# Kernel tuning notes

Hardware: AMD Instinct MI355X
Metric: run time of the kernel (lower is better)

The kernel has to match this reference:

```python
import jax, jax.numpy as jnp
import numpy as np

DT_ALPHA = 3.0
TW_ALPHA = 2.0
MAX_ITER = 5000
STOP_THR = 0.005
SINK_EPS = 1e-16
RECON_EPS = 1e-12


def pairwise_euclidean_distance(x, y):
    return jnp.sum(x * x, axis=1, keepdims=True) + jnp.sum(y * y, axis=1) - 2.0 * (x @ y.T)


def sinkhorn(M, a, b, alpha):
    # Faithful port of ETP.forward: K = exp(-alpha*M), alternating u/v scaling,
    # error checked every 50 iterations (at cpt % 50 == 1).
    K = jnp.exp(-M * alpha)
    n = a.shape[0]
    u0 = jnp.ones_like(a) / n
    v0 = jnp.zeros_like(b)

    def cond(state):
        u, v, err, cpt = state
        return (err > STOP_THR) & (cpt < MAX_ITER)

    def body(state):
        u, v, err, cpt = state
        v = b / (K.T @ u + SINK_EPS)
        u = a / (K @ v + SINK_EPS)
        cpt = cpt + 1
        err = jax.lax.cond(
            cpt % 50 == 1,
            lambda: jnp.sum(jnp.abs(v * (K.T @ u) - b)),  # inf-norm of a [1]-vector
            lambda: err,
        )
        return (u, v, err, cpt)

    u, v, _, _ = jax.lax.while_loop(
        cond, body, (u0, v0, jnp.asarray(1.0, M.dtype), jnp.asarray(0, jnp.int32))
    )
    transp = u * (K * v.T)
    loss = jnp.sum(transp * M)
    return loss, transp


def setup_inputs() -> dict:
    key = jax.random.key(0)
    kd, kw, kt, kb = jax.random.split(key, 4)
    N, V, K, E = 4096, 10000, 100, 384

    def l2norm(x):
        return x / jnp.linalg.norm(x, axis=1, keepdims=True)

    doc_embeddings = l2norm(jax.random.normal(kd, (N, E), dtype=jnp.float32))
    word_embeddings = l2norm(jax.random.normal(kw, (V, E), dtype=jnp.float32))
    topic_embeddings = l2norm(jax.random.normal(kt, (K, E), dtype=jnp.float32) * 0.1)
    train_bow = jax.random.uniform(kb, (N, V), dtype=jnp.float32)
    word_weights = jnp.ones((V, 1), dtype=jnp.float32) / V
    topic_weights = jnp.ones((K, 1), dtype=jnp.float32) / K
    return {
        "train_bow": train_bow,
        "doc_embeddings": doc_embeddings,
        "word_embeddings": word_embeddings,
        "topic_embeddings": topic_embeddings,
        "word_weights": word_weights,
        "topic_weights": topic_weights,
    }


def reference(train_bow, doc_embeddings, word_embeddings, topic_embeddings,
              word_weights, topic_weights):
    N = doc_embeddings.shape[0]
    K = topic_embeddings.shape[0]

    # Doc-Topic transport: a uniform over docs, b = softmax(topic_weights)
    M_dt = pairwise_euclidean_distance(doc_embeddings, topic_embeddings)
    a_dt = jnp.ones((N, 1), dtype=M_dt.dtype) / N
    b_dt = jax.nn.softmax(topic_weights, axis=0)
    loss_DT, transp_DT = sinkhorn(M_dt, a_dt, b_dt, DT_ALPHA)

    # Topic-Word transport: a uniform over topics, b = softmax(word_weights)
    M_tw = pairwise_euclidean_distance(topic_embeddings, word_embeddings)
    a_tw = jnp.ones((K, 1), dtype=M_tw.dtype) / K
    b_tw = jax.nn.softmax(word_weights, axis=0)
    loss_TW, transp_TW = sinkhorn(M_tw, a_tw, b_tw, TW_ALPHA)

    theta = transp_DT * N        # [N, K]
    beta = transp_TW * K         # [K, V]
    recon = theta @ beta         # [N, V]
    loss_DSR = -jnp.mean(jnp.sum(train_bow * jnp.log(recon + RECON_EPS), axis=1))
    return loss_DSR + loss_DT + loss_TW
```

## Files before the change

### kernel.cpp

```cpp
#include <hip/hip_runtime.h>

#define N_DOCS   4096
#define N_WORDS  10000
#define N_TOPICS 100
#define EDIM     384
#define KPAD     128
#define BT_ROWS  10112
#define RECON_BLOCKS (79 * 32)
#define APPLY_BLOCKS 2088

#define OFF_KDT   16u
#define OFF_KDTT  (OFF_KDT  + 409600u)
#define OFF_KTW   (OFF_KDTT + 409600u)
#define OFF_BDT   (OFF_KTW  + 1000000u)
#define OFF_BTW   (OFF_BDT  + 128u)
#define OFF_ND    (OFF_BTW  + 10016u)
#define OFF_NW    (OFF_ND   + 4096u)
#define OFF_NT    (OFF_NW   + 10016u)
#define OFF_UDT   (OFF_NT   + 128u)
#define OFF_VDT   (OFF_UDT  + 4096u)
#define OFF_UTW   (OFF_VDT  + 128u)
#define OFF_VTW   (OFF_UTW  + 128u)
#define OFF_THB   (OFF_VTW  + 10016u)
#define OFF_BTT   (OFF_THB  + 262144u)
#define OFF_RPART (OFF_BTT  + 647168u)
#define OFF_APART (OFF_RPART + 5056u)

typedef __attribute__((ext_vector_type(8))) short bf16x8;
typedef __attribute__((ext_vector_type(4))) float f32x4;

__device__ __forceinline__ float block_reduce_sum_256(float v, volatile float* sh) {
#pragma unroll
  for (int off = 32; off > 0; off >>= 1) v += __shfl_down(v, off, 64);
  __syncthreads();
  if ((threadIdx.x & 63) == 0) sh[threadIdx.x >> 6] = v;
  __syncthreads();
  return sh[0] + sh[1] + sh[2] + sh[3];
}

__device__ __forceinline__ float block_reduce_sum_1024(float v, volatile float* sh) {
#pragma unroll
  for (int off = 32; off > 0; off >>= 1) v += __shfl_down(v, off, 64);
  if ((threadIdx.x & 63) == 0) sh[threadIdx.x >> 6] = v;
  __syncthreads();
  if (threadIdx.x == 0) {
    float s = 0.f;
    for (int i = 0; i < 16; ++i) s += sh[i];
    sh[16] = s;
  }
  __syncthreads();
  float r = sh[16];
  __syncthreads();
  return r;
}

__device__ __forceinline__ float block_reduce_max_1024(float v, volatile float* sh) {
#pragma unroll
  for (int off = 32; off > 0; off >>= 1) v = fmaxf(v, __shfl_down(v, off, 64));
  if ((threadIdx.x & 63) == 0) sh[threadIdx.x >> 6] = v;
  __syncthreads();
  if (threadIdx.x == 0) {
    float m = sh[0];
    for (int i = 1; i < 16; ++i) m = fmaxf(m, sh[i]);
    sh[16] = m;
  }
  __syncthreads();
  float r = sh[16];
  __syncthreads();
  return r;
}

__device__ __forceinline__ unsigned short f2bf(float x) {
  union { float f; unsigned int u; } c; c.f = x;
  unsigned int r = c.u + 0x7FFF + ((c.u >> 16) & 1);
  return (unsigned short)(r >> 16);
}

__global__ __launch_bounds__(1024)
void prep_norms_kernel(const float* __restrict__ docs, const float* __restrict__ words,
                       const float* __restrict__ topics,
                       const float* __restrict__ topic_w, const float* __restrict__ word_w,
                       float* __restrict__ nd, float* __restrict__ nw, float* __restrict__ nt,
                       float* __restrict__ b_dt, float* __restrict__ b_tw,
                       float* __restrict__ errs) {
  int tid = threadIdx.x, lane = tid & 63, wave = tid >> 6;
  if (blockIdx.x < 888) {
    int row = blockIdx.x * 16 + wave;
    if (row < N_DOCS + N_WORDS + N_TOPICS) {
      const float* src; float* dst; int r;
      if (row < N_DOCS)                { src = docs;   r = row;                    dst = nd; }
      else if (row < N_DOCS + N_WORDS) { src = words;  r = row - N_DOCS;           dst = nw; }
      else                             { src = topics; r = row - N_DOCS - N_WORDS; dst = nt; }
      float s = 0.f;
#pragma unroll
      for (int k = lane; k < EDIM; k += 64) { float x = src[r * EDIM + k]; s += x * x; }
#pragma unroll
      for (int off = 32; off > 0; off >>= 1) s += __shfl_down(s, off, 64);
      if (lane == 0) dst[r] = s;
    }
    return;
  }
  __shared__ float sh[20];
  float m = (tid < N_TOPICS) ? topic_w[tid] : -3.0e38f;
  m = block_reduce_max_1024(m, sh);
  float e = (tid < N_TOPICS) ? __expf(topic_w[tid] - m) : 0.f;
  float s = block_reduce_sum_1024(e, sh);
  if (tid < N_TOPICS) b_dt[tid] = e / s;
  float m2 = -3.0e38f;
  for (int i = tid * 4; i < N_WORDS; i += 4096) {
    float4 w = *reinterpret_cast<const float4*>(&word_w[i]);
    m2 = fmaxf(fmaxf(m2, fmaxf(w.x, w.y)), fmaxf(w.z, w.w));
  }
  m2 = block_reduce_max_1024(m2, sh);
  float s2 = 0.f;
  for (int i = tid * 4; i < N_WORDS; i += 4096) {
    float4 w = *reinterpret_cast<const float4*>(&word_w[i]);
    s2 += __expf(w.x - m2) + __expf(w.y - m2) + __expf(w.z - m2) + __expf(w.w - m2);
  }
  s2 = block_reduce_sum_1024(s2, sh);
  float inv2 = 1.0f / s2;
  for (int i = tid * 4; i < N_WORDS; i += 4096) {
    float4 w = *reinterpret_cast<const float4*>(&word_w[i]);
    float4 o = make_float4(__expf(w.x - m2) * inv2, __expf(w.y - m2) * inv2,
                           __expf(w.z - m2) * inv2, __expf(w.w - m2) * inv2);
    *reinterpret_cast<float4*>(&b_tw[i]) = o;
  }
  if (tid < 2) errs[tid] = 0.f;
}

__global__ __launch_bounds__(256)
void dist_kernel(const float* __restrict__ docs, const float* __restrict__ words,
                 const float* __restrict__ topics,
                 const float* __restrict__ nd, const float* __restrict__ nw,
                 const float* __restrict__ nt,
                 float* __restrict__ Kdt, float* __restrict__ KdtT,
                 float* __restrict__ Ktw) {
  __shared__ __align__(16) float As[16][64];
  __shared__ __align__(16) float Bs[16][64];
  const int bid = blockIdx.x;
  const float *A, *B, *nA, *nB; float *Kout, *KoutT; int nI, nJ, i0, j0; float alpha;
  if (bid < 128) {
    A = docs; B = topics; nA = nd; nB = nt; Kout = Kdt; KoutT = KdtT;
    nI = N_DOCS; nJ = N_TOPICS; alpha = 3.0f;
    j0 = (bid & 1) * 64; i0 = (bid >> 1) * 64;
  } else {
    int b2 = bid - 128;
    A = topics; B = words; nA = nt; nB = nw; Kout = Ktw; KoutT = nullptr;
    nI = N_TOPICS; nJ = N_WORDS; alpha = 2.0f;
    i0 = (b2 & 1) * 64; j0 = (b2 >> 1) * 64;
  }
  const int tid = threadIdx.x;
  const int r = tid & 63, kg = tid >> 6;
  const int tx = tid & 15, ty = tid >> 4;
  float acc[4][4] = {};
  for (int k0 = 0; k0 < EDIM; k0 += 16) {
    float4 av = make_float4(0.f, 0.f, 0.f, 0.f);
    float4 bv = make_float4(0.f, 0.f, 0.f, 0.f);
    int gi = i0 + r, gj = j0 + r;
    if (gi < nI) av = *reinterpret_cast<const float4*>(&A[gi * EDIM + k0 + kg * 4]);
    if (gj < nJ) bv = *reinterpret_cast<const float4*>(&B[gj * EDIM + k0 + kg * 4]);
    As[kg * 4 + 0][r] = av.x; As[kg * 4 + 1][r] = av.y;
    As[kg * 4 + 2][r] = av.z; As[kg * 4 + 3][r] = av.w;
    Bs[kg * 4 + 0][r] = bv.x; Bs[kg * 4 + 1][r] = bv.y;
    Bs[kg * 4 + 2][r] = bv.z; Bs[kg * 4 + 3][r] = bv.w;
    __syncthreads();
#pragma unroll
    for (int kk = 0; kk < 16; ++kk) {
      float4 a4 = *reinterpret_cast<const float4*>(&As[kk][ty * 4]);
      float4 b4 = *reinterpret_cast<const float4*>(&Bs[kk][tx * 4]);
      float aa[4] = {a4.x, a4.y, a4.z, a4.w};
      float bb[4] = {b4.x, b4.y, b4.z, b4.w};
#pragma unroll
      for (int di = 0; di < 4; ++di)
#pragma unroll
        for (int dj = 0; dj < 4; ++dj) acc[di][dj] += aa[di] * bb[dj];
    }
    __syncthreads();
  }
#pragma unroll
  for (int di = 0; di < 4; ++di) {
    int gi = i0 + ty * 4 + di;
    if (gi < nI) {
      float na = nA[gi];
#pragma unroll
      for (int dj = 0; dj < 4; ++dj) {
        int gj = j0 + tx * 4 + dj;
        if (gj < nJ) {
          float val = __expf(-alpha * (na + nB[gj] - 2.f * acc[di][dj]));
          Kout[(size_t)gi * nJ + gj] = val;
          if (KoutT) KoutT[(size_t)gj * nI + gi] = val;
        }
      }
    }
  }
}

__global__ __launch_bounds__(256)
void cs_kernel(const float* __restrict__ KdtT, const float* __restrict__ b_dt,
               float* __restrict__ v_dt,
               const float* __restrict__ Ktw, const float* __restrict__ b_tw,
               float* __restrict__ v_tw) {
  __shared__ float sh[4];
  const int tid = threadIdx.x;
  if (blockIdx.x < 100) {
    int j = blockIdx.x;
    float s = 0.f;
#pragma unroll 8
    for (int i = tid; i < N_DOCS; i += 256) s += KdtT[(size_t)j * N_DOCS + i];
    s = block_reduce_sum_256(s, sh);
    if (tid == 0) v_dt[j] = b_dt[j] / (s * (1.0f / N_DOCS) + 1e-16f);
  } else {
    int j = (blockIdx.x - 100) * 256 + tid;
    if (j < N_WORDS) {
      float s = 0.f;
#pragma unroll 10
      for (int i = 0; i < N_TOPICS; ++i) s += Ktw[(size_t)i * N_WORDS + j];
      v_tw[j] = b_tw[j] / (s * 0.01f + 1e-16f);
    }
  }
}

__global__ __launch_bounds__(256)
void u_kernel(const float* __restrict__ Kdt, const float* __restrict__ v_dt,
              float* __restrict__ u_dt,
              const float* __restrict__ Ktw, const float* __restrict__ v_tw,
              float* __restrict__ u_tw) {
  __shared__ float vl[N_TOPICS];
  __shared__ float sh[4];
  const int tid = threadIdx.x;
  if (blockIdx.x < 16) {
    if (tid < N_TOPICS) vl[tid] = v_dt[tid];
    __syncthreads();
    int i = blockIdx.x * 256 + tid;
    float d = 0.f;
    const float* row = &Kdt[(size_t)i * N_TOPICS];
#pragma unroll
    for (int j4 = 0; j4 < N_TOPICS; j4 += 4) {
      float4 kv = *reinterpret_cast<const float4*>(&row[j4]);
      d += kv.x * vl[j4] + kv.y * vl[j4 + 1] + kv.z * vl[j4 + 2] + kv.w * vl[j4 + 3];
    }
    u_dt[i] = (1.0f / N_DOCS) / (d + 1e-16f);
  } else {
    int i = blockIdx.x - 16;
    float d = 0.f;
    const float* row = &Ktw[(size_t)i * N_WORDS];
    for (int j = tid * 4; j < N_WORDS; j += 1024) {
      float4 kv = *reinterpret_cast<const float4*>(&row[j]);
      float4 vv = *reinterpret_cast<const float4*>(&v_tw[j]);
      d += kv.x * vv.x + kv.y * vv.y + kv.z * vv.z + kv.w * vv.w;
    }
    d = block_reduce_sum_256(d, sh);
    if (tid == 0) u_tw[i] = 0.01f / (d + 1e-16f);
  }
}

__global__ __launch_bounds__(256)
void err_kernel(const float* __restrict__ KdtT, const float* __restrict__ u_dt,
                const float* __restrict__ v_dt, const float* __restrict__ b_dt,
                const float* __restrict__ Ktw, const float* __restrict__ u_tw,
                const float* __restrict__ v_tw, const float* __restrict__ b_tw,
                float* __restrict__ errs) {
  __shared__ float sh[4];
  __shared__ float ul[N_TOPICS];
  const int tid = threadIdx.x;
  if (blockIdx.x < 100) {
    int j = blockIdx.x;
    float s = 0.f;
#pragma unroll 8
    for (int i = tid; i < N_DOCS; i += 256) s += KdtT[(size_t)j * N_DOCS + i] * u_dt[i];
    s = block_reduce_sum_256(s, sh);
    if (tid == 0) atomicAdd(&errs[0], fabsf(v_dt[j] * s - b_dt[j]));
  } else {
    if (tid < N_TOPICS) ul[tid] = u_tw[tid];
    __syncthreads();
    int j = (blockIdx.x - 100) * 256 + tid;
    float e = 0.f;
    if (j < N_WORDS) {
      float s = 0.f;
#pragma unroll 10
      for (int i = 0; i < N_TOPICS; ++i) s += Ktw[(size_t)i * N_WORDS + j] * ul[i];
      e = fabsf(v_tw[j] * s - b_tw[j]);
    }
    e = block_reduce_sum_256(e, sh);
    if (tid == 0) atomicAdd(&errs[1], e);
  }
}

__global__ __launch_bounds__(1024)
void rem_kernel(const float* __restrict__ Kdt, const float* __restrict__ KdtT,
                const float* __restrict__ b_dt, float* __restrict__ u_dt,
                float* __restrict__ v_dt,
                const float* __restrict__ Ktw, const float* __restrict__ b_tw,
                float* __restrict__ u_tw, float* __restrict__ v_tw,
                const float* __restrict__ errs) {
  __shared__ float rsm[20104];
  const int tid = threadIdx.x, wave = tid >> 6, lane = tid & 63;
  if (blockIdx.x == 0) {
    float err = errs[0];
    if (!(err > 0.005f)) return;
    float* u_l = rsm; float* v_l = rsm + 4096; float* bl = rsm + 4196; float* esh = rsm + 4296;
    for (int i = tid; i < N_DOCS; i += 1024) u_l[i] = u_dt[i];
    if (tid < N_TOPICS) { bl[tid] = b_dt[tid]; v_l[tid] = v_dt[tid]; }
    __syncthreads();
    int cpt = 1;
    while (err > 0.005f && cpt < 5000) {
      for (int j = wave; j < N_TOPICS; j += 16) {
        float s = 0.f;
        for (int i = lane; i < N_DOCS; i += 64) s += KdtT[(size_t)j * N_DOCS + i] * u_l[i];
#pragma unroll
        for (int off = 32; off > 0; off >>= 1) s += __shfl_down(s, off, 64);
        if (lane == 0) v_l[j] = bl[j] / (s + 1e-16f);
      }
      __syncthreads();
      for (int i = tid; i < N_DOCS; i += 1024) {
        float d = 0.f;
        for (int j = 0; j < N_TOPICS; ++j) d += Kdt[(size_t)i * N_TOPICS + j] * v_l[j];
        u_l[i] = (1.0f / N_DOCS) / (d + 1e-16f);
      }
      __syncthreads();
      ++cpt;
      if (cpt % 50 == 1) {
        if (tid == 0) *esh = 0.f;
        __syncthreads();
        for (int j = wave; j < N_TOPICS; j += 16) {
          float s = 0.f;
          for (int i = lane; i < N_DOCS; i += 64) s += KdtT[(size_t)j * N_DOCS + i] * u_l[i];
#pragma unroll
          for (int off = 32; off > 0; off >>= 1) s += __shfl_down(s, off, 64);
          if (lane == 0) atomicAdd(esh, fabsf(v_l[j] * s - bl[j]));
        }
        __syncthreads();
        err = *esh;
        __syncthreads();
      }
    }
    for (int i = tid; i < N_DOCS; i += 1024) u_dt[i] = u_l[i];
    if (tid < N_TOPICS) v_dt[tid] = v_l[tid];
  } else {
    float err = errs[1];
    if (!(err > 0.005f)) return;
    float* v_l = rsm; float* bl = rsm + 10000; float* u_l = rsm + 20000; float* esh = rsm + 20100;
    for (int j = tid; j < N_WORDS; j += 1024) { v_l[j] = v_tw[j]; bl[j] = b_tw[j]; }
    if (tid < N_TOPICS) u_l[tid] = u_tw[tid];
    __syncthreads();
    int cpt = 1;
    while (err > 0.005f && cpt < 5000) {
      for (int j = tid; j < N_WORDS; j += 1024) {
        float s = 0.f;
        for (int i = 0; i < N_TOPICS; ++i) s += Ktw[(size_t)i * N_WORDS + j] * u_l[i];
        v_l[j] = bl[j] / (s + 1e-16f);
      }
      __syncthreads();
      for (int i = wave; i < N_TOPICS; i += 16) {
        float s = 0.f;
        for (int j = lane; j < N_WORDS; j += 64) s += Ktw[(size_t)i * N_WORDS + j] * v_l[j];
#pragma unroll
        for (int off = 32; off > 0; off >>= 1) s += __shfl_down(s, off, 64);
        if (lane == 0) u_l[i] = 0.01f / (s + 1e-16f);
      }
      __syncthreads();
      ++cpt;
      if (cpt % 50 == 1) {
        if (tid == 0) *esh = 0.f;
        __syncthreads();
        float e = 0.f;
        for (int j = tid; j < N_WORDS; j += 1024) {
          float s = 0.f;
          for (int i = 0; i < N_TOPICS; ++i) s += Ktw[(size_t)i * N_WORDS + j] * u_l[i];
          e += fabsf(v_l[j] * s - bl[j]);
        }
        atomicAdd(esh, e);
        __syncthreads();
        err = *esh;
        __syncthreads();
      }
    }
    for (int j = tid; j < N_WORDS; j += 1024) v_tw[j] = v_l[j];
    if (tid < N_TOPICS) u_tw[tid] = u_l[tid];
  }
}

__global__ __launch_bounds__(256)
void apply_kernel(const float* __restrict__ Kdt, const float* __restrict__ u_dt,
                  const float* __restrict__ v_dt,
                  const float* __restrict__ Ktw, const float* __restrict__ u_tw,
                  const float* __restrict__ v_tw,
                  unsigned short* __restrict__ theta_b, unsigned short* __restrict__ beta_bT,
                  double* __restrict__ apart) {
  __shared__ float sh[4];
  __shared__ float ul[N_TOPICS];
  const int tid = threadIdx.x;
  float lp = 0.f;
  if (blockIdx.x < 2048) {
    int idx = blockIdx.x * 256 + tid;
    int i = idx >> 7, k = idx & 127;
    unsigned short o = 0;
    if (k < N_TOPICS) {
      float kv = Kdt[(size_t)i * N_TOPICS + k];
      float t = u_dt[i] * kv * v_dt[k];
      lp = t * (-__logf(kv) * (1.0f / 3.0f));
      o = f2bf(t * (float)N_DOCS);
    }
    theta_b[idx] = o;
  } else {
    if (tid < N_TOPICS) ul[tid] = u_tw[tid];
    __syncthreads();
    int n = (blockIdx.x - 2048) * 256 + tid;
    if (n < N_WORDS) {
      float vn = v_tw[n];
      unsigned short* dst = &beta_bT[(size_t)n * KPAD];
#pragma unroll 2
      for (int kc = 0; kc < KPAD; kc += 8) {
        unsigned short pk[8];
#pragma unroll
        for (int q = 0; q < 8; ++q) {
          int k = kc + q;
          unsigned short o = 0;
          if (k < N_TOPICS) {
            float kv = Ktw[(size_t)k * N_WORDS + n];
            float t = ul[k] * kv * vn;
            lp += t * (-__logf(kv) * 0.5f);
            o = f2bf(t * (float)N_TOPICS);
          }
          pk[q] = o;
        }
        *(uint4*)&dst[kc] = *(uint4*)pk;
      }
    } else if (n < BT_ROWS) {
      unsigned short* dst = &beta_bT[(size_t)n * KPAD];
      uint4 z = make_uint4(0, 0, 0, 0);
#pragma unroll
      for (int kc = 0; kc < KPAD; kc += 8) *(uint4*)&dst[kc] = z;
    }
  }
  lp = block_reduce_sum_256(lp, sh);
  if (tid == 0) apart[blockIdx.x] = (double)lp;
}

#define AS_LD 136
#define CLD   132
__global__ __launch_bounds__(256, 2)
void recon_kernel(const unsigned short* __restrict__ theta_b,
                  const unsigned short* __restrict__ beta_bT,
                  const float* __restrict__ bow, double* __restrict__ rpart) {
  __shared__ __align__(16) char smem[128 * AS_LD * 2 * 2];
  __shared__ float sh4[4];
  unsigned short* As = (unsigned short*)smem;
  unsigned short* Bs = As + 128 * AS_LD;
  float* C = (float*)smem;
  const int tid = threadIdx.x;
  const int c0 = blockIdx.x * 128, r0 = blockIdx.y * 128;

#pragma unroll
  for (int pass = 0; pass < 8; ++pass) {
    int idx = pass * 256 + tid;
    int r = idx >> 4, k16 = idx & 15;
    *(uint4*)&As[r * AS_LD + k16 * 8] = *(const uint4*)&theta_b[(size_t)(r0 + r) * KPAD + k16 * 8];
    *(uint4*)&Bs[r * AS_LD + k16 * 8] = *(const uint4*)&beta_bT[(size_t)(c0 + r) * KPAD + k16 * 8];
  }
  __syncthreads();

  const int wave = tid >> 6, lane = tid & 63;
  const int wr = (wave >> 1) * 64, wc = (wave & 1) * 64;
  const int lm = lane & 15, q = lane >> 4;
  f32x4 acc[4][4] = {};
#pragma unroll
  for (int kc = 0; kc < 4; ++kc) {
    int k = kc * 32 + q * 8;
    bf16x8 af[4], bfr[4];
#pragma unroll
    for (int t = 0; t < 4; ++t) {
      af[t]  = *(const bf16x8*)&As[(wr + t * 16 + lm) * AS_LD + k];
      bfr[t] = *(const bf16x8*)&Bs[(wc + t * 16 + lm) * AS_LD + k];
    }
#pragma unroll
    for (int mi = 0; mi < 4; ++mi)
#pragma unroll
      for (int ni = 0; ni < 4; ++ni)
        acc[mi][ni] = __builtin_amdgcn_mfma_f32_16x16x32_bf16(af[mi], bfr[ni],
                                                              acc[mi][ni], 0, 0, 0);
  }
  __syncthreads();

#pragma unroll
  for (int mi = 0; mi < 4; ++mi)
#pragma unroll
    for (int ni = 0; ni < 4; ++ni)
#pragma unroll
      for (int reg = 0; reg < 4; ++reg) {
        int row = wr + mi * 16 + q * 4 + reg;
        int col = wc + ni * 16 + lm;
        C[row * CLD + col] = acc[mi][ni][reg];
      }
  __syncthreads();

  float lp = 0.f;
  const int c4 = tid & 31;
  const int rb = tid >> 5;
  const int gj0 = c0 + c4 * 4;
  if (gj0 < N_WORDS) {
#pragma unroll
    for (int it = 0; it < 16; ++it) {
      int row = rb + it * 8;
      float4 bw = *reinterpret_cast<const float4*>(&bow[(size_t)(r0 + row) * N_WORDS + gj0]);
      float4 rc = *reinterpret_cast<const float4*>(&C[row * CLD + c4 * 4]);
      lp += bw.x * __logf(rc.x + 1e-12f) + bw.y * __logf(rc.y + 1e-12f)
          + bw.z * __logf(rc.z + 1e-12f) + bw.w * __logf(rc.w + 1e-12f);
    }
  }
  lp = block_reduce_sum_256(lp, sh4);
  if (tid == 0) rpart[blockIdx.y * 79 + blockIdx.x] = (double)lp;
}

__global__ __launch_bounds__(1024)
void finalize_kernel(const double* __restrict__ rpart, const double* __restrict__ apart,
                     float* __restrict__ out) {
  __shared__ double sh[17];
  const int tid = threadIdx.x, lane = tid & 63;
  double s2 = 0.0, s01 = 0.0;
  for (int i = tid; i < RECON_BLOCKS; i += 1024) s2 += rpart[i];
  for (int i = tid; i < APPLY_BLOCKS; i += 1024) s01 += apart[i];
  double t = s01 - s2 * (1.0 / N_DOCS);
#pragma unroll
  for (int off = 32; off > 0; off >>= 1) t += __shfl_down(t, off, 64);
  if (lane == 0) sh[tid >> 6] = t;
  __syncthreads();
  if (tid == 0) {
    double s = 0.0;
    for (int i = 0; i < 16; ++i) s += sh[i];
    out[0] = (float)s;
  }
}

extern "C" void kernel_launch(void* const* d_in, const int* in_sizes, int n_in,
                              void* d_out, int out_size, void* d_ws, size_t ws_size,
                              hipStream_t stream) {
  const float* bow     = (const float*)d_in[0];
  const float* docs    = (const float*)d_in[1];
  const float* words   = (const float*)d_in[2];
  const float* topics  = (const float*)d_in[3];
  const float* word_w  = (const float*)d_in[4];
  const float* topic_w = (const float*)d_in[5];
  float* out = (float*)d_out;

  float* fws  = (float*)d_ws;
  float* errs = fws + 8;
  float* Kdt  = fws + OFF_KDT;
  float* KdtT = fws + OFF_KDTT;
  float* Ktw  = fws + OFF_KTW;
  float* b_dt = fws + OFF_BDT;
  float* b_tw = fws + OFF_BTW;
  float* nd   = fws + OFF_ND;
  float* nw   = fws + OFF_NW;
  float* nt   = fws + OFF_NT;
  float* u_dt = fws + OFF_UDT;
  float* v_dt = fws + OFF_VDT;
  float* u_tw = fws + OFF_UTW;
  float* v_tw = fws + OFF_VTW;
  unsigned short* theta_b = (unsigned short*)(fws + OFF_THB);
  unsigned short* beta_bT = (unsigned short*)(fws + OFF_BTT);
  double* rpart = (double*)(fws + OFF_RPART);
  double* apart = (double*)(fws + OFF_APART);

  prep_norms_kernel<<<dim3(889), dim3(1024), 0, stream>>>(
      docs, words, topics, topic_w, word_w, nd, nw, nt, b_dt, b_tw, errs);
  dist_kernel<<<dim3(442), dim3(256), 0, stream>>>(
      docs, words, topics, nd, nw, nt, Kdt, KdtT, Ktw);
  cs_kernel<<<dim3(140), dim3(256), 0, stream>>>(KdtT, b_dt, v_dt, Ktw, b_tw, v_tw);
  u_kernel<<<dim3(116), dim3(256), 0, stream>>>(Kdt, v_dt, u_dt, Ktw, v_tw, u_tw);
  err_kernel<<<dim3(140), dim3(256), 0, stream>>>(
      KdtT, u_dt, v_dt, b_dt, Ktw, u_tw, v_tw, b_tw, errs);
  rem_kernel<<<dim3(2), dim3(1024), 0, stream>>>(
      Kdt, KdtT, b_dt, u_dt, v_dt, Ktw, b_tw, u_tw, v_tw, errs);
  apply_kernel<<<dim3(APPLY_BLOCKS), dim3(256), 0, stream>>>(
      Kdt, u_dt, v_dt, Ktw, u_tw, v_tw, theta_b, beta_bT, apart);
  recon_kernel<<<dim3(79, 32), dim3(256), 0, stream>>>(theta_b, beta_bT, bow, rpart);
  finalize_kernel<<<dim3(1), dim3(1024), 0, stream>>>(rpart, apart, out);

  (void)in_sizes; (void)n_in; (void)out_size; (void)ws_size;
}
```

Baseline: 368.4 us.

## Fuse Sinkhorn stages into a cooperative kernel and compute distances with bf16 MFMA

The separate norm and softmax prep kernel is removed. Row norms are now computed inside the distance kernel, and the softmax weights are computed inside the Sinkhorn kernel. The distance GEMM switches from fp32 FMA tiling to bf16 MFMA, and the four Sinkhorn launches (column sums, u update, error check, remaining iterations) become one cooperative kernel separated by grid.sync. This is meant to cut launch overhead and an extra pass over the embeddings. In exchange, the dot products are computed in bf16, which adds error before the exponential. The iterative remainder loop now runs with 256 instead of 1024 threads per block, which could slow it down if many iterations execute.

```diff
diff --git a/kernel.cpp b/kernel.cpp
--- a/kernel.cpp
+++ b/kernel.cpp
@@ -1,4 +1,7 @@
 #include <hip/hip_runtime.h>
+#include <hip/hip_cooperative_groups.h>
+
+namespace cg = cooperative_groups;
 
 #define N_DOCS   4096
 #define N_WORDS  10000
@@ -14,10 +17,7 @@
 #define OFF_KTW   (OFF_KDTT + 409600u)
 #define OFF_BDT   (OFF_KTW  + 1000000u)
 #define OFF_BTW   (OFF_BDT  + 128u)
-#define OFF_ND    (OFF_BTW  + 10016u)
-#define OFF_NW    (OFF_ND   + 4096u)
-#define OFF_NT    (OFF_NW   + 10016u)
-#define OFF_UDT   (OFF_NT   + 128u)
+#define OFF_UDT   (OFF_BTW  + 10016u)
 #define OFF_VDT   (OFF_UDT  + 4096u)
 #define OFF_UTW   (OFF_VDT  + 128u)
 #define OFF_VTW   (OFF_UTW  + 128u)
@@ -38,36 +38,13 @@
   return sh[0] + sh[1] + sh[2] + sh[3];
 }
 
-__device__ __forceinline__ float block_reduce_sum_1024(float v, volatile float* sh) {
-#pragma unroll
-  for (int off = 32; off > 0; off >>= 1) v += __shfl_down(v, off, 64);
+__device__ __forceinline__ float block_reduce_max_256(float v, volatile float* sh) {
+#pragma unroll
+  for (int off = 32; off > 0; off >>= 1) v = fmaxf(v, __shfl_down(v, off, 64));
+  __syncthreads();
   if ((threadIdx.x & 63) == 0) sh[threadIdx.x >> 6] = v;
   __syncthreads();
-  if (threadIdx.x == 0) {
-    float s = 0.f;
-    for (int i = 0; i < 16; ++i) s += sh[i];
-    sh[16] = s;
-  }
-  __syncthreads();
-  float r = sh[16];
-  __syncthreads();
-  return r;
-}
-
-__device__ __forceinline__ float block_reduce_max_1024(float v, volatile float* sh) {
-#pragma unroll
-  for (int off = 32; off > 0; off >>= 1) v = fmaxf(v, __shfl_down(v, off, 64));
-  if ((threadIdx.x & 63) == 0) sh[threadIdx.x >> 6] = v;
-  __syncthreads();
-  if (threadIdx.x == 0) {
-    float m = sh[0];
-    for (int i = 1; i < 16; ++i) m = fmaxf(m, sh[i]);
-    sh[16] = m;
-  }
-  __syncthreads();
-  float r = sh[16];
-  __syncthreads();
-  return r;
+  return fmaxf(fmaxf(sh[0], sh[1]), fmaxf(sh[2], sh[3]));
 }
 
 __device__ __forceinline__ unsigned short f2bf(float x) {
@@ -76,204 +53,181 @@
   return (unsigned short)(r >> 16);
 }
 
-__global__ __launch_bounds__(1024)
-void prep_norms_kernel(const float* __restrict__ docs, const float* __restrict__ words,
-                       const float* __restrict__ topics,
-                       const float* __restrict__ topic_w, const float* __restrict__ word_w,
-                       float* __restrict__ nd, float* __restrict__ nw, float* __restrict__ nt,
-                       float* __restrict__ b_dt, float* __restrict__ b_tw,
-                       float* __restrict__ errs) {
-  int tid = threadIdx.x, lane = tid & 63, wave = tid >> 6;
-  if (blockIdx.x < 888) {
-    int row = blockIdx.x * 16 + wave;
-    if (row < N_DOCS + N_WORDS + N_TOPICS) {
-      const float* src; float* dst; int r;
-      if (row < N_DOCS)                { src = docs;   r = row;                    dst = nd; }
-      else if (row < N_DOCS + N_WORDS) { src = words;  r = row - N_DOCS;           dst = nw; }
-      else                             { src = topics; r = row - N_DOCS - N_WORDS; dst = nt; }
-      float s = 0.f;
-#pragma unroll
-      for (int k = lane; k < EDIM; k += 64) { float x = src[r * EDIM + k]; s += x * x; }
-#pragma unroll
-      for (int off = 32; off > 0; off >>= 1) s += __shfl_down(s, off, 64);
-      if (lane == 0) dst[r] = s;
-    }
-    return;
-  }
-  __shared__ float sh[20];
-  float m = (tid < N_TOPICS) ? topic_w[tid] : -3.0e38f;
-  m = block_reduce_max_1024(m, sh);
-  float e = (tid < N_TOPICS) ? __expf(topic_w[tid] - m) : 0.f;
-  float s = block_reduce_sum_1024(e, sh);
-  if (tid < N_TOPICS) b_dt[tid] = e / s;
-  float m2 = -3.0e38f;
-  for (int i = tid * 4; i < N_WORDS; i += 4096) {
-    float4 w = *reinterpret_cast<const float4*>(&word_w[i]);
-    m2 = fmaxf(fmaxf(m2, fmaxf(w.x, w.y)), fmaxf(w.z, w.w));
-  }
-  m2 = block_reduce_max_1024(m2, sh);
-  float s2 = 0.f;
-  for (int i = tid * 4; i < N_WORDS; i += 4096) {
-    float4 w = *reinterpret_cast<const float4*>(&word_w[i]);
-    s2 += __expf(w.x - m2) + __expf(w.y - m2) + __expf(w.z - m2) + __expf(w.w - m2);
-  }
-  s2 = block_reduce_sum_1024(s2, sh);
-  float inv2 = 1.0f / s2;
-  for (int i = tid * 4; i < N_WORDS; i += 4096) {
-    float4 w = *reinterpret_cast<const float4*>(&word_w[i]);
-    float4 o = make_float4(__expf(w.x - m2) * inv2, __expf(w.y - m2) * inv2,
-                           __expf(w.z - m2) * inv2, __expf(w.w - m2) * inv2);
-    *reinterpret_cast<float4*>(&b_tw[i]) = o;
-  }
-  if (tid < 2) errs[tid] = 0.f;
-}
-
+#define DLD 40
 __global__ __launch_bounds__(256)
 void dist_kernel(const float* __restrict__ docs, const float* __restrict__ words,
                  const float* __restrict__ topics,
-                 const float* __restrict__ nd, const float* __restrict__ nw,
-                 const float* __restrict__ nt,
                  float* __restrict__ Kdt, float* __restrict__ KdtT,
                  float* __restrict__ Ktw) {
-  __shared__ __align__(16) float As[16][64];
-  __shared__ __align__(16) float Bs[16][64];
-  const int bid = blockIdx.x;
-  const float *A, *B, *nA, *nB; float *Kout, *KoutT; int nI, nJ, i0, j0; float alpha;
+  __shared__ __align__(16) unsigned short Abf[64 * DLD];
+  __shared__ __align__(16) unsigned short Bbf[64 * DLD];
+  __shared__ float na[64], nb[64];
+  const int bid = blockIdx.x, tid = threadIdx.x;
+  const float *A, *B; float *Kout, *KoutT; int nI, nJ, i0, j0; float alpha;
   if (bid < 128) {
-    A = docs; B = topics; nA = nd; nB = nt; Kout = Kdt; KoutT = KdtT;
+    A = docs; B = topics; Kout = Kdt; KoutT = KdtT;
     nI = N_DOCS; nJ = N_TOPICS; alpha = 3.0f;
     j0 = (bid & 1) * 64; i0 = (bid >> 1) * 64;
   } else {
     int b2 = bid - 128;
-    A = topics; B = words; nA = nt; nB = nw; Kout = Ktw; KoutT = nullptr;
+    A = topics; B = words; Kout = Ktw; KoutT = nullptr;
     nI = N_TOPICS; nJ = N_WORDS; alpha = 2.0f;
     i0 = (b2 & 1) * 64; j0 = (b2 >> 1) * 64;
   }
-  const int tid = threadIdx.x;
-  const int r = tid & 63, kg = tid >> 6;
-  const int tx = tid & 15, ty = tid >> 4;
-  float acc[4][4] = {};
-  for (int k0 = 0; k0 < EDIM; k0 += 16) {
-    float4 av = make_float4(0.f, 0.f, 0.f, 0.f);
-    float4 bv = make_float4(0.f, 0.f, 0.f, 0.f);
-    int gi = i0 + r, gj = j0 + r;
-    if (gi < nI) av = *reinterpret_cast<const float4*>(&A[gi * EDIM + k0 + kg * 4]);
-    if (gj < nJ) bv = *reinterpret_cast<const float4*>(&B[gj * EDIM + k0 + kg * 4]);
-    As[kg * 4 + 0][r] = av.x; As[kg * 4 + 1][r] = av.y;
-    As[kg * 4 + 2][r] = av.z; As[kg * 4 + 3][r] = av.w;
-    Bs[kg * 4 + 0][r] = bv.x; Bs[kg * 4 + 1][r] = bv.y;
-    Bs[kg * 4 + 2][r] = bv.z; Bs[kg * 4 + 3][r] = bv.w;
-    __syncthreads();
-#pragma unroll
-    for (int kk = 0; kk < 16; ++kk) {
-      float4 a4 = *reinterpret_cast<const float4*>(&As[kk][ty * 4]);
-      float4 b4 = *reinterpret_cast<const float4*>(&Bs[kk][tx * 4]);
-      float aa[4] = {a4.x, a4.y, a4.z, a4.w};
-      float bb[4] = {b4.x, b4.y, b4.z, b4.w};
-#pragma unroll
-      for (int di = 0; di < 4; ++di)
-#pragma unroll
-        for (int dj = 0; dj < 4; ++dj) acc[di][dj] += aa[di] * bb[dj];
-    }
-    __syncthreads();
-  }
-#pragma unroll
-  for (int di = 0; di < 4; ++di) {
-    int gi = i0 + ty * 4 + di;
-    if (gi < nI) {
-      float na = nA[gi];
-#pragma unroll
-      for (int dj = 0; dj < 4; ++dj) {
-        int gj = j0 + tx * 4 + dj;
-        if (gj < nJ) {
-          float val = __expf(-alpha * (na + nB[gj] - 2.f * acc[di][dj]));
-          Kout[(size_t)gi * nJ + gj] = val;
-          if (KoutT) KoutT[(size_t)gj * nI + gi] = val;
-        }
+  const int rs = tid >> 3, c4 = tid & 7;
+  const int giA0 = i0 + rs, giA1 = i0 + rs + 32;
+  const int gjB0 = j0 + rs, gjB1 = j0 + rs + 32;
+  const int wave = tid >> 6, lane = tid & 63, lm = lane & 15, q = lane >> 4;
+  const int wr = wave * 16;
+  float ssA0 = 0.f, ssA1 = 0.f, ssB0 = 0.f, ssB1 = 0.f;
+  f32x4 acc[4] = {};
+  for (int kc = 0; kc < 12; ++kc) {
+    const int kb = kc * 32 + c4 * 4;
+    float4 a0 = make_float4(0.f, 0.f, 0.f, 0.f), a1 = a0, b0 = a0, b1 = a0;
+    if (giA0 < nI) a0 = *(const float4*)&A[(size_t)giA0 * EDIM + kb];
+    if (giA1 < nI) a1 = *(const float4*)&A[(size_t)giA1 * EDIM + kb];
+    if (gjB0 < nJ) b0 = *(const float4*)&B[(size_t)gjB0 * EDIM + kb];
+    if (gjB1 < nJ) b1 = *(const float4*)&B[(size_t)gjB1 * EDIM + kb];
+    ssA0 += a0.x * a0.x + a0.y * a0.y + a0.z * a0.z + a0.w * a0.w;
+    ssA1 += a1.x * a1.x + a1.y * a1.y + a1.z * a1.z + a1.w * a1.w;
+    ssB0 += b0.x * b0.x + b0.y * b0.y + b0.z * b0.z + b0.w * b0.w;
+    ssB1 += b1.x * b1.x + b1.y * b1.y + b1.z * b1.z + b1.w * b1.w;
+    ushort4 pa0 = make_ushort4(f2bf(a0.x), f2bf(a0.y), f2bf(a0.z), f2bf(a0.w));
+    ushort4 pa1 = make_ushort4(f2bf(a1.x), f2bf(a1.y), f2bf(a1.z), f2bf(a1.w));
+    ushort4 pb0 = make_ushort4(f2bf(b0.x), f2bf(b0.y), f2bf(b0.z), f2bf(b0.w));
+    ushort4 pb1 = make_ushort4(f2bf(b1.x), f2bf(b1.y), f2bf(b1.z), f2bf(b1.w));
+    __syncthreads();
+    *(ushort4*)&Abf[rs * DLD + c4 * 4]        = pa0;
+    *(ushort4*)&Abf[(rs + 32) * DLD + c4 * 4] = pa1;
+    *(ushort4*)&Bbf[rs * DLD + c4 * 4]        = pb0;
+    *(ushort4*)&Bbf[(rs + 32) * DLD + c4 * 4] = pb1;
+    __syncthreads();
+    bf16x8 af = *(const bf16x8*)&Abf[(wr + lm) * DLD + q * 8];
+#pragma unroll
+    for (int ni = 0; ni < 4; ++ni) {
+      bf16x8 bf = *(const bf16x8*)&Bbf[(ni * 16 + lm) * DLD + q * 8];
+      acc[ni] = __builtin_amdgcn_mfma_f32_16x16x32_bf16(af, bf, acc[ni], 0, 0, 0);
+    }
+  }
+  ssA0 += __shfl_down(ssA0, 4); ssA0 += __shfl_down(ssA0, 2); ssA0 += __shfl_down(ssA0, 1);
+  ssA1 += __shfl_down(ssA1, 4); ssA1 += __shfl_down(ssA1, 2); ssA1 += __shfl_down(ssA1, 1);
+  ssB0 += __shfl_down(ssB0, 4); ssB0 += __shfl_down(ssB0, 2); ssB0 += __shfl_down(ssB0, 1);
+  ssB1 += __shfl_down(ssB1, 4); ssB1 += __shfl_down(ssB1, 2); ssB1 += __shfl_down(ssB1, 1);
+  __syncthreads();
+  if ((tid & 7) == 0) {
+    na[rs] = ssA0; na[rs + 32] = ssA1;
+    nb[rs] = ssB0; nb[rs + 32] = ssB1;
+  }
+  __syncthreads();
+#pragma unroll
+  for (int ni = 0; ni < 4; ++ni) {
+    int col = ni * 16 + lm, gj = j0 + col;
+#pragma unroll
+    for (int reg = 0; reg < 4; ++reg) {
+      int row = wr + q * 4 + reg, gi = i0 + row;
+      if (gi < nI && gj < nJ) {
+        float d = na[row] + nb[col] - 2.f * acc[ni][reg];
+        float val = __expf(-alpha * d);
+        Kout[(size_t)gi * nJ + gj] = val;
+        if (KoutT) KoutT[(size_t)gj * nI + gi] = val;
       }
     }
   }
 }
 
 __global__ __launch_bounds__(256)
-void cs_kernel(const float* __restrict__ KdtT, const float* __restrict__ b_dt,
-               float* __restrict__ v_dt,
-               const float* __restrict__ Ktw, const float* __restrict__ b_tw,
-               float* __restrict__ v_tw) {
-  __shared__ float sh[4];
-  const int tid = threadIdx.x;
-  if (blockIdx.x < 100) {
-    int j = blockIdx.x;
+void sinkhorn_kernel(const float* __restrict__ Kdt, const float* __restrict__ KdtT,
+                     const float* __restrict__ Ktw,
+                     const float* __restrict__ topic_w, const float* __restrict__ word_w,
+                     float* __restrict__ b_dt, float* __restrict__ b_tw,
+                     float* __restrict__ u_dt, float* __restrict__ v_dt,
+                     float* __restrict__ u_tw, float* __restrict__ v_tw,
+                     float* __restrict__ errs) {
+  cg::grid_group grid = cg::this_grid();
+  __shared__ float rsm[20104];
+  const int bid = blockIdx.x, tid = threadIdx.x;
+  const int wave = tid >> 6, lane = tid & 63;
+
+  if (bid < 100) {
+    int j = bid;
+    float m = (tid < N_TOPICS) ? topic_w[tid] : -3.0e38f;
+    m = block_reduce_max_256(m, rsm);
+    float e = (tid < N_TOPICS) ? __expf(topic_w[tid] - m) : 0.f;
+    float S = block_reduce_sum_256(e, rsm);
     float s = 0.f;
 #pragma unroll 8
     for (int i = tid; i < N_DOCS; i += 256) s += KdtT[(size_t)j * N_DOCS + i];
-    s = block_reduce_sum_256(s, sh);
-    if (tid == 0) v_dt[j] = b_dt[j] / (s * (1.0f / N_DOCS) + 1e-16f);
+    s = block_reduce_sum_256(s, rsm);
+    if (tid == 0) {
+      float bj = __expf(topic_w[j] - m) / S;
+      b_dt[j] = bj;
+      v_dt[j] = bj / (s * (1.0f / N_DOCS) + 1e-16f);
+      if (j == 0) { errs[0] = 0.f; errs[1] = 0.f; }
+    }
   } else {
-    int j = (blockIdx.x - 100) * 256 + tid;
+    float m2 = -3.0e38f;
+    for (int i = tid * 4; i < N_WORDS; i += 1024) {
+      float4 w = *(const float4*)&word_w[i];
+      m2 = fmaxf(fmaxf(m2, fmaxf(w.x, w.y)), fmaxf(w.z, w.w));
+    }
+    m2 = block_reduce_max_256(m2, rsm);
+    float s2 = 0.f;
+    for (int i = tid * 4; i < N_WORDS; i += 1024) {
+      float4 w = *(const float4*)&word_w[i];
+      s2 += __expf(w.x - m2) + __expf(w.y - m2) + __expf(w.z - m2) + __expf(w.w - m2);
+    }
+    s2 = block_reduce_sum_256(s2, rsm);
+    int j = (bid - 100) * 256 + tid;
     if (j < N_WORDS) {
       float s = 0.f;
 #pragma unroll 10
       for (int i = 0; i < N_TOPICS; ++i) s += Ktw[(size_t)i * N_WORDS + j];
-      v_tw[j] = b_tw[j] / (s * 0.01f + 1e-16f);
-    }
-  }
-}
-
-__global__ __launch_bounds__(256)
-void u_kernel(const float* __restrict__ Kdt, const float* __restrict__ v_dt,
-              float* __restrict__ u_dt,
-              const float* __restrict__ Ktw, const float* __restrict__ v_tw,
-              float* __restrict__ u_tw) {
-  __shared__ float vl[N_TOPICS];
-  __shared__ float sh[4];
-  const int tid = threadIdx.x;
-  if (blockIdx.x < 16) {
+      float bj = __expf(word_w[j] - m2) / s2;
+      b_tw[j] = bj;
+      v_tw[j] = bj / (s * 0.01f + 1e-16f);
+    }
+  }
+  grid.sync();
+
+  if (bid < 16) {
+    float* vl = rsm + 4;
     if (tid < N_TOPICS) vl[tid] = v_dt[tid];
     __syncthreads();
-    int i = blockIdx.x * 256 + tid;
+    int i = bid * 256 + tid;
     float d = 0.f;
     const float* row = &Kdt[(size_t)i * N_TOPICS];
 #pragma unroll
     for (int j4 = 0; j4 < N_TOPICS; j4 += 4) {
-      float4 kv = *reinterpret_cast<const float4*>(&row[j4]);
+      float4 kv = *(const float4*)&row[j4];
       d += kv.x * vl[j4] + kv.y * vl[j4 + 1] + kv.z * vl[j4 + 2] + kv.w * vl[j4 + 3];
     }
     u_dt[i] = (1.0f / N_DOCS) / (d + 1e-16f);
-  } else {
-    int i = blockIdx.x - 16;
+  } else if (bid < 116) {
+    int i = bid - 16;
     float d = 0.f;
     const float* row = &Ktw[(size_t)i * N_WORDS];
     for (int j = tid * 4; j < N_WORDS; j += 1024) {
-      float4 kv = *reinterpret_cast<const float4*>(&row[j]);
-      float4 vv = *reinterpret_cast<const float4*>(&v_tw[j]);
+      float4 kv = *(const float4*)&row[j];
+      float4 vv = *(const float4*)&v_tw[j];
       d += kv.x * vv.x + kv.y * vv.y + kv.z * vv.z + kv.w * vv.w;
     }
-    d = block_reduce_sum_256(d, sh);
+    d = block_reduce_sum_256(d, rsm);
     if (tid == 0) u_tw[i] = 0.01f / (d + 1e-16f);
   }
-}
-
-__global__ __launch_bounds__(256)
-void err_kernel(const float* __restrict__ KdtT, const float* __restrict__ u_dt,
-                const float* __restrict__ v_dt, const float* __restrict__ b_dt,
-                const float* __restrict__ Ktw, const float* __restrict__ u_tw,
-                const float* __restrict__ v_tw, const float* __restrict__ b_tw,
-                float* __restrict__ errs) {
-  __shared__ float sh[4];
-  __shared__ float ul[N_TOPICS];
-  const int tid = threadIdx.x;
-  if (blockIdx.x < 100) {
-    int j = blockIdx.x;
+  grid.sync();
+
+  if (bid < 100) {
+    int j = bid;
     float s = 0.f;
 #pragma unroll 8
     for (int i = tid; i < N_DOCS; i += 256) s += KdtT[(size_t)j * N_DOCS + i] * u_dt[i];
-    s = block_reduce_sum_256(s, sh);
+    s = block_reduce_sum_256(s, rsm);
     if (tid == 0) atomicAdd(&errs[0], fabsf(v_dt[j] * s - b_dt[j]));
   } else {
+    float* ul = rsm + 4;
     if (tid < N_TOPICS) ul[tid] = u_tw[tid];
     __syncthreads();
-    int j = (blockIdx.x - 100) * 256 + tid;
+    int j = (bid - 100) * 256 + tid;
     float e = 0.f;
     if (j < N_WORDS) {
       float s = 0.f;
@@ -281,30 +235,21 @@
       for (int i = 0; i < N_TOPICS; ++i) s += Ktw[(size_t)i * N_WORDS + j] * ul[i];
       e = fabsf(v_tw[j] * s - b_tw[j]);
     }
-    e = block_reduce_sum_256(e, sh);
+    e = block_reduce_sum_256(e, rsm);
     if (tid == 0) atomicAdd(&errs[1], e);
   }
-}
-
-__global__ __launch_bounds__(1024)
-void rem_kernel(const float* __restrict__ Kdt, const float* __restrict__ KdtT,
-                const float* __restrict__ b_dt, float* __restrict__ u_dt,
-                float* __restrict__ v_dt,
-                const float* __restrict__ Ktw, const float* __restrict__ b_tw,
-                float* __restrict__ u_tw, float* __restrict__ v_tw,
-                const float* __restrict__ errs) {
-  __shared__ float rsm[20104];
-  const int tid = threadIdx.x, wave = tid >> 6, lane = tid & 63;
-  if (blockIdx.x == 0) {
+  grid.sync();
+
+  if (bid == 0) {
     float err = errs[0];
     if (!(err > 0.005f)) return;
     float* u_l = rsm; float* v_l = rsm + 4096; float* bl = rsm + 4196; float* esh = rsm + 4296;
-    for (int i = tid; i < N_DOCS; i += 1024) u_l[i] = u_dt[i];
+    for (int i = tid; i < N_DOCS; i += 256) u_l[i] = u_dt[i];
     if (tid < N_TOPICS) { bl[tid] = b_dt[tid]; v_l[tid] = v_dt[tid]; }
     __syncthreads();
     int cpt = 1;
     while (err > 0.005f && cpt < 5000) {
-      for (int j = wave; j < N_TOPICS; j += 16) {
+      for (int j = wave; j < N_TOPICS; j += 4) {
         float s = 0.f;
         for (int i = lane; i < N_DOCS; i += 64) s += KdtT[(size_t)j * N_DOCS + i] * u_l[i];
 #pragma unroll
@@ -312,7 +257,7 @@
         if (lane == 0) v_l[j] = bl[j] / (s + 1e-16f);
       }
       __syncthreads();
-      for (int i = tid; i < N_DOCS; i += 1024) {
+      for (int i = tid; i < N_DOCS; i += 256) {
         float d = 0.f;
         for (int j = 0; j < N_TOPICS; ++j) d += Kdt[(size_t)i * N_TOPICS + j] * v_l[j];
         u_l[i] = (1.0f / N_DOCS) / (d + 1e-16f);
@@ -322,7 +267,7 @@
       if (cpt % 50 == 1) {
         if (tid == 0) *esh = 0.f;
         __syncthreads();
-        for (int j = wave; j < N_TOPICS; j += 16) {
+        for (int j = wave; j < N_TOPICS; j += 4) {
           float s = 0.f;
           for (int i = lane; i < N_DOCS; i += 64) s += KdtT[(size_t)j * N_DOCS + i] * u_l[i];
 #pragma unroll
@@ -334,24 +279,24 @@
         __syncthreads();
       }
     }
-    for (int i = tid; i < N_DOCS; i += 1024) u_dt[i] = u_l[i];
+    for (int i = tid; i < N_DOCS; i += 256) u_dt[i] = u_l[i];
     if (tid < N_TOPICS) v_dt[tid] = v_l[tid];
-  } else {
+  } else if (bid == 1) {
     float err = errs[1];
     if (!(err > 0.005f)) return;
     float* v_l = rsm; float* bl = rsm + 10000; float* u_l = rsm + 20000; float* esh = rsm + 20100;
-    for (int j = tid; j < N_WORDS; j += 1024) { v_l[j] = v_tw[j]; bl[j] = b_tw[j]; }
+    for (int j = tid; j < N_WORDS; j += 256) { v_l[j] = v_tw[j]; bl[j] = b_tw[j]; }
     if (tid < N_TOPICS) u_l[tid] = u_tw[tid];
     __syncthreads();
     int cpt = 1;
     while (err > 0.005f && cpt < 5000) {
-      for (int j = tid; j < N_WORDS; j += 1024) {
+      for (int j = tid; j < N_WORDS; j += 256) {
         float s = 0.f;
         for (int i = 0; i < N_TOPICS; ++i) s += Ktw[(size_t)i * N_WORDS + j] * u_l[i];
         v_l[j] = bl[j] / (s + 1e-16f);
       }
       __syncthreads();
-      for (int i = wave; i < N_TOPICS; i += 16) {
+      for (int i = wave; i < N_TOPICS; i += 4) {
         float s = 0.f;
         for (int j = lane; j < N_WORDS; j += 64) s += Ktw[(size_t)i * N_WORDS + j] * v_l[j];
 #pragma unroll
@@ -364,7 +309,7 @@
         if (tid == 0) *esh = 0.f;
         __syncthreads();
         float e = 0.f;
-        for (int j = tid; j < N_WORDS; j += 1024) {
+        for (int j = tid; j < N_WORDS; j += 256) {
           float s = 0.f;
           for (int i = 0; i < N_TOPICS; ++i) s += Ktw[(size_t)i * N_WORDS + j] * u_l[i];
           e += fabsf(v_l[j] * s - bl[j]);
@@ -375,7 +320,7 @@
         __syncthreads();
       }
     }
-    for (int j = tid; j < N_WORDS; j += 1024) v_tw[j] = v_l[j];
+    for (int j = tid; j < N_WORDS; j += 256) v_tw[j] = v_l[j];
     if (tid < N_TOPICS) u_tw[tid] = u_l[tid];
   }
 }
@@ -450,7 +395,6 @@
   float* C = (float*)smem;
   const int tid = threadIdx.x;
   const int c0 = blockIdx.x * 128, r0 = blockIdx.y * 128;
-
 #pragma unroll
   for (int pass = 0; pass < 8; ++pass) {
     int idx = pass * 256 + tid;
@@ -459,7 +403,6 @@
     *(uint4*)&Bs[r * AS_LD + k16 * 8] = *(const uint4*)&beta_bT[(size_t)(c0 + r) * KPAD + k16 * 8];
   }
   __syncthreads();
-
   const int wave = tid >> 6, lane = tid & 63;
   const int wr = (wave >> 1) * 64, wc = (wave & 1) * 64;
   const int lm = lane & 15, q = lane >> 4;
@@ -481,7 +424,6 @@
                                                               acc[mi][ni], 0, 0, 0);
   }
   __syncthreads();
-
 #pragma unroll
   for (int mi = 0; mi < 4; ++mi)
 #pragma unroll
@@ -493,7 +435,6 @@
         C[row * CLD + col] = acc[mi][ni][reg];
       }
   __syncthreads();
-
   float lp = 0.f;
   const int c4 = tid & 31;
   const int rb = tid >> 5;
@@ -550,9 +491,6 @@
   float* Ktw  = fws + OFF_KTW;
   float* b_dt = fws + OFF_BDT;
   float* b_tw = fws + OFF_BTW;
-  float* nd   = fws + OFF_ND;
-  float* nw   = fws + OFF_NW;
-  float* nt   = fws + OFF_NT;
   float* u_dt = fws + OFF_UDT;
   float* v_dt = fws + OFF_VDT;
   float* u_tw = fws + OFF_UTW;
@@ -562,16 +500,12 @@
   double* rpart = (double*)(fws + OFF_RPART);
   double* apart = (double*)(fws + OFF_APART);
 
-  prep_norms_kernel<<<dim3(889), dim3(1024), 0, stream>>>(
-      docs, words, topics, topic_w, word_w, nd, nw, nt, b_dt, b_tw, errs);
-  dist_kernel<<<dim3(442), dim3(256), 0, stream>>>(
-      docs, words, topics, nd, nw, nt, Kdt, KdtT, Ktw);
-  cs_kernel<<<dim3(140), dim3(256), 0, stream>>>(KdtT, b_dt, v_dt, Ktw, b_tw, v_tw);
-  u_kernel<<<dim3(116), dim3(256), 0, stream>>>(Kdt, v_dt, u_dt, Ktw, v_tw, u_tw);
-  err_kernel<<<dim3(140), dim3(256), 0, stream>>>(
-      KdtT, u_dt, v_dt, b_dt, Ktw, u_tw, v_tw, b_tw, errs);
-  rem_kernel<<<dim3(2), dim3(1024), 0, stream>>>(
-      Kdt, KdtT, b_dt, u_dt, v_dt, Ktw, b_tw, u_tw, v_tw, errs);
+  dist_kernel<<<dim3(442), dim3(256), 0, stream>>>(docs, words, topics, Kdt, KdtT, Ktw);
+  {
+    void* args[] = {&Kdt, &KdtT, &Ktw, &topic_w, &word_w, &b_dt, &b_tw,
+                    &u_dt, &v_dt, &u_tw, &v_tw, &errs};
+    hipLaunchCooperativeKernel((void*)sinkhorn_kernel, dim3(140), dim3(256), args, 0, stream);
+  }
   apply_kernel<<<dim3(APPLY_BLOCKS), dim3(256), 0, stream>>>(
       Kdt, u_dt, v_dt, Ktw, u_tw, v_tw, theta_b, beta_bT, apart);
   recon_kernel<<<dim3(79, 32), dim3(256), 0, stream>>>(theta_b, beta_bT, bow, rpart);
```

Result: slower. 420.4 us (+14.1%).
